# Optimization experiments

Hardware: AMD Instinct MI355X
Metric: run time of the kernel (lower is better)

## Reference

```python
import jax, jax.numpy as jnp
import numpy as np

EMBED_DIM = 1024
NUM_HEADS = 16
HEAD_DIM = EMBED_DIM // NUM_HEADS
B, S = 4, 2048


def setup_inputs() -> dict:
    key = jax.random.key(0)
    ks = jax.random.split(key, 12)
    s = 1.0 / np.sqrt(EMBED_DIM)
    inp = {
        'q': jax.random.normal(ks[0], (B, S, EMBED_DIM), jnp.float32),
        'k': jax.random.normal(ks[1], (B, S, EMBED_DIM), jnp.float32),
        'v': jax.random.normal(ks[2], (B, S, EMBED_DIM), jnp.float32),
        'mask': jnp.tril(jnp.ones((S, S), jnp.int32))[None, None],  # [1,1,S,S] causal
        'Wq': jax.random.normal(ks[3], (EMBED_DIM, EMBED_DIM), jnp.float32) * s,
        'bq': jax.random.normal(ks[4], (EMBED_DIM,), jnp.float32) * s,
        'Wk': jax.random.normal(ks[5], (EMBED_DIM, EMBED_DIM), jnp.float32) * s,
        'bk': jax.random.normal(ks[6], (EMBED_DIM,), jnp.float32) * s,
        'Wv': jax.random.normal(ks[7], (EMBED_DIM, EMBED_DIM), jnp.float32) * s,
        'bv': jax.random.normal(ks[8], (EMBED_DIM,), jnp.float32) * s,
        'Wo': jax.random.normal(ks[9], (EMBED_DIM, EMBED_DIM), jnp.float32) * s,
        'bo': jax.random.normal(ks[10], (EMBED_DIM,), jnp.float32) * s,
    }
    return inp


def _split(x):
    b, s, _ = x.shape
    return x.reshape(b, s, NUM_HEADS, HEAD_DIM).transpose(0, 2, 1, 3)  # [b,h,s,d]


def reference(q, k, v, mask, Wq, bq, Wk, bk, Wv, bv, Wo, bo):
    # torch Linear: x @ W.T + b
    Q = _split(q @ Wq.T + bq)
    K = _split(k @ Wk.T + bk)
    V = _split(v @ Wv.T + bv)
    scores = jnp.einsum('bhqd,bhkd->bhqk', Q, K) / np.sqrt(HEAD_DIM).astype(np.float32)
    scores = jnp.where(mask == 0, jnp.float32(-1e9), scores)
    attn = jax.nn.softmax(scores, axis=-1)  # dropout p=0.0 -> identity
    out = jnp.einsum('bhqk,bhkd->bhqd', attn, V)
    out = out.transpose(0, 2, 1, 3).reshape(q.shape[0], q.shape[1], EMBED_DIM)
    return out @ Wo.T + bo
```

## Files before the change

### kernel.cpp

```cpp
#include <hip/hip_runtime.h>

#define SEQ   2048
#define EMB   1024
#define NH    16
#define HD    64
#define BATCH 4

typedef __attribute__((ext_vector_type(8))) short short8;
typedef __attribute__((ext_vector_type(4))) float floatx4;

static __device__ __forceinline__ ushort f2bf_rne(float x) {
  unsigned u = __float_as_uint(x);
  unsigned r = u + 0x7FFFu + ((u >> 16) & 1u);
  return (ushort)(r >> 16);
}
static __device__ __forceinline__ float bf2f(ushort h) {
  return __uint_as_float(((unsigned)h) << 16);
}

static __device__ __forceinline__ void load16(const void* g, void* l) {
  __builtin_amdgcn_global_load_lds(
      (const __attribute__((address_space(1))) unsigned int*)g,
      (__attribute__((address_space(3))) unsigned int*)l, 16, 0, 0);
}

static __device__ __forceinline__ int swz_off(int row, int kg) {
  return (row >> 1) * 128 + (((row & 1) << 2) + (kg ^ ((row >> 1) & 3))) * 16;
}

static __device__ __forceinline__ void stage_tile(const ushort* __restrict__ g,
                                                  int row0, int k0,
                                                  ushort* lds, int t) {
#pragma unroll
  for (int i = 0; i < 2; ++i) {
    const int slot = t + i * 256;
    const int line = slot >> 3, s = slot & 7;
    const int row = line * 2 + (s >> 2);
    const int c = (s & 3) ^ (line & 3);
    load16(g + (size_t)(row0 + row) * EMB + k0 + c * 8, lds + slot * 8);
  }
}

__global__ __launch_bounds__(256) void wconv_kernel(const float* __restrict__ W,
                                                    ushort* __restrict__ Yh,
                                                    ushort* __restrict__ Yl) {
  const int i = (blockIdx.x * 256 + threadIdx.x) * 8;
  const float4 a = *(const float4*)(W + i);
  const float4 b = *(const float4*)(W + i + 4);
  const float xv[8] = {a.x, a.y, a.z, a.w, b.x, b.y, b.z, b.w};
  uint4 hp, lp;
  uint hw[8], lw[8];
#pragma unroll
  for (int j = 0; j < 8; ++j) {
    const ushort hh = f2bf_rne(xv[j]);
    hw[j] = hh;
    lw[j] = f2bf_rne(xv[j] - bf2f(hh));
  }
  hp.x = hw[0] | (hw[1] << 16); hp.y = hw[2] | (hw[3] << 16);
  hp.z = hw[4] | (hw[5] << 16); hp.w = hw[6] | (hw[7] << 16);
  lp.x = lw[0] | (lw[1] << 16); lp.y = lw[2] | (lw[3] << 16);
  lp.z = lw[4] | (lw[5] << 16); lp.w = lw[6] | (lw[7] << 16);
  *(uint4*)&Yh[i] = hp;
  *(uint4*)&Yl[i] = lp;
}

template <int MODE, bool PREA, bool PREB>
__global__ __launch_bounds__(256) void proj_mfma_kernel(
    const float* __restrict__ X, const ushort* __restrict__ Xh,
    const ushort* __restrict__ Xl, const float* __restrict__ W,
    const ushort* __restrict__ Wh, const ushort* __restrict__ Wl,
    const float* __restrict__ bias, float* __restrict__ Yf,
    ushort* __restrict__ Yh, ushort* __restrict__ Yl) {
  __shared__ ushort Ahi[PREA ? 128 * 32 : 128 * 40];
  __shared__ ushort Alo[PREA ? 128 * 32 : 128 * 40];
  __shared__ ushort Bhi[PREB ? 128 * 32 : 128 * 40];
  __shared__ ushort Blo[PREB ? 128 * 32 : 128 * 40];

  const int t = threadIdx.x;
  const int lane = t & 63, wave = t >> 6;
  const int m0 = blockIdx.y * 128, n0 = blockIdx.x * 128;
  const int wm = (wave >> 1) * 64, wn = (wave & 1) * 64;
  const int fr = lane & 15, kg = lane >> 4;

  floatx4 acc[4][4];
#pragma unroll
  for (int i = 0; i < 4; ++i)
#pragma unroll
    for (int j = 0; j < 4; ++j)
#pragma unroll
      for (int r = 0; r < 4; ++r) acc[i][j][r] = 0.f;

#pragma unroll 1
  for (int k0 = 0; k0 < EMB; k0 += 32) {
    __syncthreads();
    if constexpr (PREA) {
      stage_tile(Xh, m0, k0, Ahi, t);
      stage_tile(Xl, m0, k0, Alo, t);
    } else {
#pragma unroll
      for (int i = 0; i < 4; ++i) {
        const int f = t + 256 * i;
        const int row = f >> 3, kq = f & 7;
        const float4 a =
            *(const float4*)(X + (size_t)(m0 + row) * EMB + k0 + kq * 4);
        const ushort h0 = f2bf_rne(a.x), h1 = f2bf_rne(a.y);
        const ushort h2 = f2bf_rne(a.z), h3 = f2bf_rne(a.w);
        const ushort l0 = f2bf_rne(a.x - bf2f(h0)), l1 = f2bf_rne(a.y - bf2f(h1));
        const ushort l2 = f2bf_rne(a.z - bf2f(h2)), l3 = f2bf_rne(a.w - bf2f(h3));
        uint2 hp, lp;
        hp.x = (uint)h0 | ((uint)h1 << 16);
        hp.y = (uint)h2 | ((uint)h3 << 16);
        lp.x = (uint)l0 | ((uint)l1 << 16);
        lp.y = (uint)l2 | ((uint)l3 << 16);
        *(uint2*)&Ahi[row * 40 + kq * 4] = hp;
        *(uint2*)&Alo[row * 40 + kq * 4] = lp;
      }
    }
    if constexpr (PREB) {
      stage_tile(Wh, n0, k0, Bhi, t);
      stage_tile(Wl, n0, k0, Blo, t);
    } else {
#pragma unroll
      for (int i = 0; i < 4; ++i) {
        const int f = t + 256 * i;
        const int row = f >> 3, kq = f & 7;
        const float4 b =
            *(const float4*)(W + (size_t)(n0 + row) * EMB + k0 + kq * 4);
        const ushort h0 = f2bf_rne(b.x), h1 = f2bf_rne(b.y);
        const ushort h2 = f2bf_rne(b.z), h3 = f2bf_rne(b.w);
        const ushort l0 = f2bf_rne(b.x - bf2f(h0)), l1 = f2bf_rne(b.y - bf2f(h1));
        const ushort l2 = f2bf_rne(b.z - bf2f(h2)), l3 = f2bf_rne(b.w - bf2f(h3));
        uint2 hp, lp;
        hp.x = (uint)h0 | ((uint)h1 << 16);
        hp.y = (uint)h2 | ((uint)h3 << 16);
        lp.x = (uint)l0 | ((uint)l1 << 16);
        lp.y = (uint)l2 | ((uint)l3 << 16);
        *(uint2*)&Bhi[row * 40 + kq * 4] = hp;
        *(uint2*)&Blo[row * 40 + kq * 4] = lp;
      }
    }
    if constexpr (PREA || PREB) asm volatile("s_waitcnt vmcnt(0)");
    __syncthreads();

    short8 bhv[4], blv[4];
#pragma unroll
    for (int nf = 0; nf < 4; ++nf) {
      const int row = wn + nf * 16 + fr;
      if constexpr (PREB) {
        const int off = swz_off(row, kg);
        bhv[nf] = *(const short8*)((const char*)Bhi + off);
        blv[nf] = *(const short8*)((const char*)Blo + off);
      } else {
        bhv[nf] = *(const short8*)&Bhi[row * 40 + kg * 8];
        blv[nf] = *(const short8*)&Blo[row * 40 + kg * 8];
      }
    }
#pragma unroll
    for (int mf = 0; mf < 4; ++mf) {
      const int arow = wm + mf * 16 + fr;
      short8 ah, al;
      if constexpr (PREA) {
        const int off = swz_off(arow, kg);
        ah = *(const short8*)((const char*)Ahi + off);
        al = *(const short8*)((const char*)Alo + off);
      } else {
        ah = *(const short8*)&Ahi[arow * 40 + kg * 8];
        al = *(const short8*)&Alo[arow * 40 + kg * 8];
      }
#pragma unroll
      for (int nf = 0; nf < 4; ++nf) {
        acc[mf][nf] = __builtin_amdgcn_mfma_f32_16x16x32_bf16(ah, bhv[nf],
                                                              acc[mf][nf], 0, 0, 0);
        acc[mf][nf] = __builtin_amdgcn_mfma_f32_16x16x32_bf16(ah, blv[nf],
                                                              acc[mf][nf], 0, 0, 0);
        acc[mf][nf] = __builtin_amdgcn_mfma_f32_16x16x32_bf16(al, bhv[nf],
                                                              acc[mf][nf], 0, 0, 0);
      }
    }
  }

  const int rg = lane >> 4;
#pragma unroll
  for (int nf = 0; nf < 4; ++nf) {
    const int n = n0 + wn + nf * 16 + fr;
    const float bb = bias[n];
    if (MODE == 2) {
      const int hh = n >> 6, d = n & 63;
#pragma unroll
      for (int mf = 0; mf < 4; ++mf) {
        const int mb = m0 + wm + mf * 16 + rg * 4;
        const int b = mb >> 11, s = mb & (SEQ - 1);
        ushort4 hv, lv;
        {
          float v0 = acc[mf][nf][0] + bb, v1 = acc[mf][nf][1] + bb;
          float v2 = acc[mf][nf][2] + bb, v3 = acc[mf][nf][3] + bb;
          hv.x = f2bf_rne(v0); lv.x = f2bf_rne(v0 - bf2f(hv.x));
          hv.y = f2bf_rne(v1); lv.y = f2bf_rne(v1 - bf2f(hv.y));
          hv.z = f2bf_rne(v2); lv.z = f2bf_rne(v2 - bf2f(hv.z));
          hv.w = f2bf_rne(v3); lv.w = f2bf_rne(v3 - bf2f(hv.w));
        }
        const int idx = (b * NH + hh) * (HD * SEQ) + d * SEQ + s;
        *(ushort4*)&Yh[idx] = hv;
        *(ushort4*)&Yl[idx] = lv;
      }
    } else {
#pragma unroll
      for (int mf = 0; mf < 4; ++mf) {
#pragma unroll
        for (int r = 0; r < 4; ++r) {
          const int m = m0 + wm + mf * 16 + rg * 4 + r;
          float val = acc[mf][nf][r] + bb;
          if (MODE == 3) {
            Yf[(size_t)m * EMB + n] = val;
          } else {
            if (MODE == 0) val *= 0.125f;
            const int hh = n >> 6, d = n & 63;
            const int b = m >> 11, s = m & (SEQ - 1);
            const int idx = ((b * NH + hh) * SEQ + s) * HD + d;
            const ushort h = f2bf_rne(val);
            Yh[idx] = h;
            Yl[idx] = f2bf_rne(val - bf2f(h));
          }
        }
      }
    }
  }
}

template <bool SPLITOUT>
__global__ __launch_bounds__(256, 2) void attn_mfma_kernel(
    const ushort* __restrict__ Qh, const ushort* __restrict__ Ql,
    const ushort* __restrict__ Kh, const ushort* __restrict__ Kl,
    const ushort* __restrict__ Vth, const ushort* __restrict__ Vtl,
    float* __restrict__ O, ushort* __restrict__ Oh, ushort* __restrict__ Ol) {
  __shared__ __align__(16) ushort KHs[64 * 64], KLs[64 * 64];
  __shared__ __align__(16) ushort VHs[64 * 64], VLs[64 * 64];
  __shared__ __align__(16) ushort Phi[128 * 72], Plo[128 * 72];

  const int bh = blockIdx.x;
  const int qt = (gridDim.y - 1) - blockIdx.y;
  const int t = threadIdx.x;
  const int lane = t & 63, wave = t >> 6;
  const int fr = lane & 15, kg = lane >> 4;
  const int base = bh * (SEQ * HD);
  const int q0 = qt * 128 + wave * 32;

  short8 qh[2][2], ql[2][2];
#pragma unroll
  for (int mf = 0; mf < 2; ++mf)
#pragma unroll
    for (int ks = 0; ks < 2; ++ks) {
      const int idx = base + (q0 + mf * 16 + fr) * HD + ks * 32 + kg * 8;
      qh[mf][ks] = *(const short8*)&Qh[idx];
      ql[mf][ks] = *(const short8*)&Ql[idx];
    }

  floatx4 oacc[2][4];
  float m_run[2][4], l_run[2][4];
#pragma unroll
  for (int mf = 0; mf < 2; ++mf) {
#pragma unroll
    for (int nf = 0; nf < 4; ++nf)
#pragma unroll
      for (int r = 0; r < 4; ++r) oacc[mf][nf][r] = 0.f;
#pragma unroll
    for (int r = 0; r < 4; ++r) {
      m_run[mf][r] = -INFINITY;
      l_run[mf][r] = 0.f;
    }
  }

  const int nkt = 2 * qt + 2;
  const int r8 = lane >> 3, c8 = lane & 7;

#pragma unroll 1
  for (int kt = 0; kt < nkt; ++kt) {
    const int c0 = kt * 64;
    __syncthreads();

#pragma unroll
    for (int i = 0; i < 2; ++i) {
      const int row = wave * 16 + i * 8 + r8;
      const int sw = ((c8 ^ (row & 7)) << 3);
      const int gk = base + (c0 + row) * HD + sw;
      const int gv = base + row * SEQ + c0 + sw;
      ushort* lk = (ushort*)((char*)KHs + (wave * 16 + i * 8) * 128);
      ushort* lkl = (ushort*)((char*)KLs + (wave * 16 + i * 8) * 128);
      ushort* lv = (ushort*)((char*)VHs + (wave * 16 + i * 8) * 128);
      ushort* lvl = (ushort*)((char*)VLs + (wave * 16 + i * 8) * 128);
      load16(Kh + gk, lk);
      load16(Kl + gk, lkl);
      load16(Vth + gv, lv);
      load16(Vtl + gv, lvl);
    }
    asm volatile("s_waitcnt vmcnt(0)");
    __syncthreads();

    if (c0 > q0 + 31) continue;

    floatx4 s[2][4];
#pragma unroll
    for (int mf = 0; mf < 2; ++mf)
#pragma unroll
      for (int nf = 0; nf < 4; ++nf)
#pragma unroll
        for (int r = 0; r < 4; ++r) s[mf][nf][r] = 0.f;

#pragma unroll
    for (int ks = 0; ks < 2; ++ks)
#pragma unroll
      for (int nf = 0; nf < 4; ++nf) {
        const int row = nf * 16 + fr;
        const int byo = row * 128 + (((ks * 4 + kg) ^ (row & 7)) << 4);
        const short8 kh = *(const short8*)((const char*)KHs + byo);
        const short8 kl = *(const short8*)((const char*)KLs + byo);
#pragma unroll
        for (int mf = 0; mf < 2; ++mf) {
          s[mf][nf] = __builtin_amdgcn_mfma_f32_16x16x32_bf16(
              qh[mf][ks], kh, s[mf][nf], 0, 0, 0);
          s[mf][nf] = __builtin_amdgcn_mfma_f32_16x16x32_bf16(
              qh[mf][ks], kl, s[mf][nf], 0, 0, 0);
          s[mf][nf] = __builtin_amdgcn_mfma_f32_16x16x32_bf16(
              ql[mf][ks], kh, s[mf][nf], 0, 0, 0);
        }
      }

    if (c0 + 63 > q0) {
#pragma unroll
      for (int mf = 0; mf < 2; ++mf)
#pragma unroll
        for (int nf = 0; nf < 4; ++nf)
#pragma unroll
          for (int r = 0; r < 4; ++r) {
            const int row = q0 + mf * 16 + kg * 4 + r;
            const int col = c0 + nf * 16 + fr;
            if (col > row) s[mf][nf][r] = -1e9f;
          }
    }

#pragma unroll
    for (int mf = 0; mf < 2; ++mf)
#pragma unroll
      for (int r = 0; r < 4; ++r) {
        float v0 = s[mf][0][r], v1 = s[mf][1][r];
        float v2 = s[mf][2][r], v3 = s[mf][3][r];
        float tm = fmaxf(fmaxf(v0, v1), fmaxf(v2, v3));
        tm = fmaxf(tm, __shfl_xor(tm, 1));
        tm = fmaxf(tm, __shfl_xor(tm, 2));
        tm = fmaxf(tm, __shfl_xor(tm, 4));
        tm = fmaxf(tm, __shfl_xor(tm, 8));
        const float mnew = fmaxf(m_run[mf][r], tm);
        const float alpha = __expf(m_run[mf][r] - mnew);
        m_run[mf][r] = mnew;
        const float p0 = __expf(v0 - mnew), p1 = __expf(v1 - mnew);
        const float p2 = __expf(v2 - mnew), p3 = __expf(v3 - mnew);
        float rs = p0 + p1 + p2 + p3;
        rs += __shfl_xor(rs, 1);
        rs += __shfl_xor(rs, 2);
        rs += __shfl_xor(rs, 4);
        rs += __shfl_xor(rs, 8);
        l_run[mf][r] = l_run[mf][r] * alpha + rs;
        const int qrow = wave * 32 + mf * 16 + kg * 4 + r;
        const float pv[4] = {p0, p1, p2, p3};
#pragma unroll
        for (int nf = 0; nf < 4; ++nf) {
          const ushort h = f2bf_rne(pv[nf]);
          Phi[qrow * 72 + nf * 16 + fr] = h;
          Plo[qrow * 72 + nf * 16 + fr] = f2bf_rne(pv[nf] - bf2f(h));
        }
#pragma unroll
        for (int nf = 0; nf < 4; ++nf) oacc[mf][nf][r] *= alpha;
      }

#pragma unroll
    for (int ks = 0; ks < 2; ++ks) {
      short8 ph[2], pl[2];
#pragma unroll
      for (int mf = 0; mf < 2; ++mf) {
        const int qrow = wave * 32 + mf * 16 + fr;
        ph[mf] = *(const short8*)&Phi[qrow * 72 + ks * 32 + kg * 8];
        pl[mf] = *(const short8*)&Plo[qrow * 72 + ks * 32 + kg * 8];
      }
#pragma unroll
      for (int nf = 0; nf < 4; ++nf) {
        const int d = nf * 16 + fr;
        const int byo = d * 128 + (((ks * 4 + kg) ^ (d & 7)) << 4);
        const short8 vh = *(const short8*)((const char*)VHs + byo);
        const short8 vl = *(const short8*)((const char*)VLs + byo);
#pragma unroll
        for (int mf = 0; mf < 2; ++mf) {
          oacc[mf][nf] = __builtin_amdgcn_mfma_f32_16x16x32_bf16(
              ph[mf], vh, oacc[mf][nf], 0, 0, 0);
          oacc[mf][nf] = __builtin_amdgcn_mfma_f32_16x16x32_bf16(
              ph[mf], vl, oacc[mf][nf], 0, 0, 0);
          oacc[mf][nf] = __builtin_amdgcn_mfma_f32_16x16x32_bf16(
              pl[mf], vh, oacc[mf][nf], 0, 0, 0);
        }
      }
    }
  }

  const int b = bh >> 4, hsel = bh & 15;
#pragma unroll
  for (int mf = 0; mf < 2; ++mf)
#pragma unroll
    for (int r = 0; r < 4; ++r) {
      const int grow = q0 + mf * 16 + kg * 4 + r;
      const float inv = 1.f / l_run[mf][r];
      const int rowbase = (b * SEQ + grow) * EMB + hsel * HD;
#pragma unroll
      for (int nf = 0; nf < 4; ++nf) {
        const float val = oacc[mf][nf][r] * inv;
        const int idx = rowbase + nf * 16 + fr;
        if constexpr (SPLITOUT) {
          const ushort hh = f2bf_rne(val);
          Oh[idx] = hh;
          Ol[idx] = f2bf_rne(val - bf2f(hh));
        } else {
          O[idx] = val;
        }
      }
    }
}

extern "C" void kernel_launch(void* const* d_in, const int* in_sizes, int n_in,
                              void* d_out, int out_size, void* d_ws,
                              size_t ws_size, hipStream_t stream) {
  const float* q = (const float*)d_in[0];
  const float* k = (const float*)d_in[1];
  const float* v = (const float*)d_in[2];
  const float* Wq = (const float*)d_in[4];
  const float* bq = (const float*)d_in[5];
  const float* Wk = (const float*)d_in[6];
  const float* bk = (const float*)d_in[7];
  const float* Wv = (const float*)d_in[8];
  const float* bv = (const float*)d_in[9];
  const float* Wo = (const float*)d_in[10];
  const float* bo = (const float*)d_in[11];
  float* out = (float*)d_out;

  const size_t E = (size_t)BATCH * SEQ * EMB;
  const size_t WE = (size_t)EMB * EMB;
  ushort* us = (ushort*)d_ws;
  ushort* Qh = us;
  ushort* Ql = us + E;
  ushort* Kh = us + 2 * E;
  ushort* Kl = us + 3 * E;
  ushort* Vth = us + 4 * E;
  ushort* Vtl = us + 5 * E;

  const dim3 pgrid(EMB / 128, (BATCH * SEQ) / 128);
  const dim3 agrid(BATCH * NH, SEQ / 128);
  const dim3 blk(256);
  const int wgrid = (int)(WE / 8 / 256);

  if (ws_size >= 8 * E * sizeof(ushort)) {
    ushort* W3 = us + 6 * E;
    ushort* Wqh = W3, *Wql = W3 + WE;
    ushort* Wkh = W3 + 2 * WE, *Wkl = W3 + 3 * WE;
    ushort* Wvh = W3 + 4 * WE, *Wvl = W3 + 5 * WE;
    ushort* AOh = us + 6 * E, *AOl = us + 7 * E;
    ushort* Woh = us, *Wol = us + WE;

    wconv_kernel<<<wgrid, blk, 0, stream>>>(Wq, Wqh, Wql);
    wconv_kernel<<<wgrid, blk, 0, stream>>>(Wk, Wkh, Wkl);
    wconv_kernel<<<wgrid, blk, 0, stream>>>(Wv, Wvh, Wvl);
    proj_mfma_kernel<0, false, true><<<pgrid, blk, 0, stream>>>(
        q, nullptr, nullptr, nullptr, Wqh, Wql, bq, nullptr, Qh, Ql);
    proj_mfma_kernel<1, false, true><<<pgrid, blk, 0, stream>>>(
        k, nullptr, nullptr, nullptr, Wkh, Wkl, bk, nullptr, Kh, Kl);
    proj_mfma_kernel<2, false, true><<<pgrid, blk, 0, stream>>>(
        v, nullptr, nullptr, nullptr, Wvh, Wvl, bv, nullptr, Vth, Vtl);
    attn_mfma_kernel<true><<<agrid, blk, 0, stream>>>(Qh, Ql, Kh, Kl, Vth, Vtl,
                                                      nullptr, AOh, AOl);
    wconv_kernel<<<wgrid, blk, 0, stream>>>(Wo, Woh, Wol);
    proj_mfma_kernel<3, true, true><<<pgrid, blk, 0, stream>>>(
        nullptr, AOh, AOl, nullptr, Woh, Wol, bo, out, nullptr, nullptr);
  } else if (ws_size >= (6 * E + 6 * WE) * sizeof(ushort)) {
    ushort* W3 = us + 6 * E;
    ushort* Wqh = W3, *Wql = W3 + WE;
    ushort* Wkh = W3 + 2 * WE, *Wkl = W3 + 3 * WE;
    ushort* Wvh = W3 + 4 * WE, *Wvl = W3 + 5 * WE;
    ushort* AOh = (ushort*)d_out, *AOl = AOh + E;
    ushort* Woh = us, *Wol = us + WE;
    float* PO = (float*)(us + 2 * E);

    wconv_kernel<<<wgrid, blk, 0, stream>>>(Wq, Wqh, Wql);
    wconv_kernel<<<wgrid, blk, 0, stream>>>(Wk, Wkh, Wkl);
    wconv_kernel<<<wgrid, blk, 0, stream>>>(Wv, Wvh, Wvl);
    proj_mfma_kernel<0, false, true><<<pgrid, blk, 0, stream>>>(
        q, nullptr, nullptr, nullptr, Wqh, Wql, bq, nullptr, Qh, Ql);
    proj_mfma_kernel<1, false, true><<<pgrid, blk, 0, stream>>>(
        k, nullptr, nullptr, nullptr, Wkh, Wkl, bk, nullptr, Kh, Kl);
    proj_mfma_kernel<2, false, true><<<pgrid, blk, 0, stream>>>(
        v, nullptr, nullptr, nullptr, Wvh, Wvl, bv, nullptr, Vth, Vtl);
    attn_mfma_kernel<true><<<agrid, blk, 0, stream>>>(Qh, Ql, Kh, Kl, Vth, Vtl,
                                                      nullptr, AOh, AOl);
    wconv_kernel<<<wgrid, blk, 0, stream>>>(Wo, Woh, Wol);
    proj_mfma_kernel<3, true, true><<<pgrid, blk, 0, stream>>>(
        nullptr, AOh, AOl, nullptr, Woh, Wol, bo, PO, nullptr, nullptr);
    hipMemcpyAsync(out, PO, E * sizeof(float), hipMemcpyDeviceToDevice, stream);
  } else {
    float* AO = out;
    float* PO = (float*)d_ws;
    proj_mfma_kernel<0, false, false><<<pgrid, blk, 0, stream>>>(
        q, nullptr, nullptr, Wq, nullptr, nullptr, bq, nullptr, Qh, Ql);
    proj_mfma_kernel<1, false, false><<<pgrid, blk, 0, stream>>>(
        k, nullptr, nullptr, Wk, nullptr, nullptr, bk, nullptr, Kh, Kl);
    proj_mfma_kernel<2, false, false><<<pgrid, blk, 0, stream>>>(
        v, nullptr, nullptr, Wv, nullptr, nullptr, bv, nullptr, Vth, Vtl);
    attn_mfma_kernel<false><<<agrid, blk, 0, stream>>>(
        Qh, Ql, Kh, Kl, Vth, Vtl, AO, nullptr, nullptr);
    proj_mfma_kernel<3, false, false><<<pgrid, blk, 0, stream>>>(
        AO, nullptr, nullptr, Wo, nullptr, nullptr, bo, PO, nullptr, nullptr);
    hipMemcpyAsync(out, PO, E * sizeof(float), hipMemcpyDeviceToDevice, stream);
  }
}
```

Before: 438.4 us.

## Compute transposed S tile so P stays in registers, drop LDS P staging

```diff
diff --git a/kernel.cpp b/kernel.cpp
--- a/kernel.cpp
+++ b/kernel.cpp
@@ -228,14 +228,13 @@
 }
 
 template <bool SPLITOUT>
-__global__ __launch_bounds__(256, 2) void attn_mfma_kernel(
+__global__ __launch_bounds__(256, 4) void attn_mfma_kernel(
     const ushort* __restrict__ Qh, const ushort* __restrict__ Ql,
     const ushort* __restrict__ Kh, const ushort* __restrict__ Kl,
     const ushort* __restrict__ Vth, const ushort* __restrict__ Vtl,
     float* __restrict__ O, ushort* __restrict__ Oh, ushort* __restrict__ Ol) {
   __shared__ __align__(16) ushort KHs[64 * 64], KLs[64 * 64];
   __shared__ __align__(16) ushort VHs[64 * 64], VLs[64 * 64];
-  __shared__ __align__(16) ushort Phi[128 * 72], Plo[128 * 72];
 
   const int bh = blockIdx.x;
   const int qt = (gridDim.y - 1) - blockIdx.y;
@@ -256,18 +255,15 @@
     }
 
   floatx4 oacc[2][4];
-  float m_run[2][4], l_run[2][4];
+  float m_run[2], l_run[2];
 #pragma unroll
   for (int mf = 0; mf < 2; ++mf) {
 #pragma unroll
     for (int nf = 0; nf < 4; ++nf)
 #pragma unroll
       for (int r = 0; r < 4; ++r) oacc[mf][nf][r] = 0.f;
-#pragma unroll
-    for (int r = 0; r < 4; ++r) {
-      m_run[mf][r] = -INFINITY;
-      l_run[mf][r] = 0.f;
-    }
+    m_run[mf] = -INFINITY;
+    l_run[mf] = 0.f;
   }
 
   const int nkt = 2 * qt + 2;
@@ -298,30 +294,30 @@
 
     if (c0 > q0 + 31) continue;
 
-    floatx4 s[2][4];
+    floatx4 s2[2][4];
 #pragma unroll
     for (int mf = 0; mf < 2; ++mf)
 #pragma unroll
       for (int nf = 0; nf < 4; ++nf)
 #pragma unroll
-        for (int r = 0; r < 4; ++r) s[mf][nf][r] = 0.f;
-
-#pragma unroll
-    for (int ks = 0; ks < 2; ++ks)
+        for (int r = 0; r < 4; ++r) s2[mf][nf][r] = 0.f;
+
+#pragma unroll
+    for (int ksd = 0; ksd < 2; ++ksd)
 #pragma unroll
       for (int nf = 0; nf < 4; ++nf) {
-        const int row = nf * 16 + fr;
-        const int byo = row * 128 + (((ks * 4 + kg) ^ (row & 7)) << 4);
+        const int kr = 32 * (nf >> 1) + 8 * (fr >> 2) + 4 * (nf & 1) + (fr & 3);
+        const int byo = kr * 128 + (((ksd * 4 + kg) ^ (kr & 7)) << 4);
         const short8 kh = *(const short8*)((const char*)KHs + byo);
         const short8 kl = *(const short8*)((const char*)KLs + byo);
 #pragma unroll
         for (int mf = 0; mf < 2; ++mf) {
-          s[mf][nf] = __builtin_amdgcn_mfma_f32_16x16x32_bf16(
-              qh[mf][ks], kh, s[mf][nf], 0, 0, 0);
-          s[mf][nf] = __builtin_amdgcn_mfma_f32_16x16x32_bf16(
-              qh[mf][ks], kl, s[mf][nf], 0, 0, 0);
-          s[mf][nf] = __builtin_amdgcn_mfma_f32_16x16x32_bf16(
-              ql[mf][ks], kh, s[mf][nf], 0, 0, 0);
+          s2[mf][nf] = __builtin_amdgcn_mfma_f32_16x16x32_bf16(
+              kh, qh[mf][ksd], s2[mf][nf], 0, 0, 0);
+          s2[mf][nf] = __builtin_amdgcn_mfma_f32_16x16x32_bf16(
+              kh, ql[mf][ksd], s2[mf][nf], 0, 0, 0);
+          s2[mf][nf] = __builtin_amdgcn_mfma_f32_16x16x32_bf16(
+              kl, qh[mf][ksd], s2[mf][nf], 0, 0, 0);
         }
       }
 
@@ -332,55 +328,68 @@
         for (int nf = 0; nf < 4; ++nf)
 #pragma unroll
           for (int r = 0; r < 4; ++r) {
-            const int row = q0 + mf * 16 + kg * 4 + r;
-            const int col = c0 + nf * 16 + fr;
-            if (col > row) s[mf][nf][r] = -1e9f;
+            const int col = c0 + 32 * (nf >> 1) + 8 * kg + 4 * (nf & 1) + r;
+            const int row = q0 + mf * 16 + fr;
+            if (col > row) s2[mf][nf][r] = -1e9f;
           }
     }
 
+    float alpha2[2];
+#pragma unroll
+    for (int mf = 0; mf < 2; ++mf) {
+      float pm = s2[mf][0][0];
+#pragma unroll
+      for (int nf = 0; nf < 4; ++nf)
+#pragma unroll
+        for (int r = 0; r < 4; ++r) pm = fmaxf(pm, s2[mf][nf][r]);
+      pm = fmaxf(pm, __shfl_xor(pm, 16));
+      pm = fmaxf(pm, __shfl_xor(pm, 32));
+      const float mnew = fmaxf(m_run[mf], pm);
+      const float al = __expf(m_run[mf] - mnew);
+      m_run[mf] = mnew;
+      float sum = 0.f;
+#pragma unroll
+      for (int nf = 0; nf < 4; ++nf)
+#pragma unroll
+        for (int r = 0; r < 4; ++r) {
+          const float p = __expf(s2[mf][nf][r] - mnew);
+          s2[mf][nf][r] = p;
+          sum += p;
+        }
+      sum += __shfl_xor(sum, 16);
+      sum += __shfl_xor(sum, 32);
+      l_run[mf] = l_run[mf] * al + sum;
+      alpha2[mf] = al;
+    }
+
 #pragma unroll
     for (int mf = 0; mf < 2; ++mf)
 #pragma unroll
       for (int r = 0; r < 4; ++r) {
-        float v0 = s[mf][0][r], v1 = s[mf][1][r];
-        float v2 = s[mf][2][r], v3 = s[mf][3][r];
-        float tm = fmaxf(fmaxf(v0, v1), fmaxf(v2, v3));
-        tm = fmaxf(tm, __shfl_xor(tm, 1));
-        tm = fmaxf(tm, __shfl_xor(tm, 2));
-        tm = fmaxf(tm, __shfl_xor(tm, 4));
-        tm = fmaxf(tm, __shfl_xor(tm, 8));
-        const float mnew = fmaxf(m_run[mf][r], tm);
-        const float alpha = __expf(m_run[mf][r] - mnew);
-        m_run[mf][r] = mnew;
-        const float p0 = __expf(v0 - mnew), p1 = __expf(v1 - mnew);
-        const float p2 = __expf(v2 - mnew), p3 = __expf(v3 - mnew);
-        float rs = p0 + p1 + p2 + p3;
-        rs += __shfl_xor(rs, 1);
-        rs += __shfl_xor(rs, 2);
-        rs += __shfl_xor(rs, 4);
-        rs += __shfl_xor(rs, 8);
-        l_run[mf][r] = l_run[mf][r] * alpha + rs;
-        const int qrow = wave * 32 + mf * 16 + kg * 4 + r;
-        const float pv[4] = {p0, p1, p2, p3};
-#pragma unroll
-        for (int nf = 0; nf < 4; ++nf) {
-          const ushort h = f2bf_rne(pv[nf]);
-          Phi[qrow * 72 + nf * 16 + fr] = h;
-          Plo[qrow * 72 + nf * 16 + fr] = f2bf_rne(pv[nf] - bf2f(h));
-        }
-#pragma unroll
-        for (int nf = 0; nf < 4; ++nf) oacc[mf][nf][r] *= alpha;
-      }
-
-#pragma unroll
-    for (int ks = 0; ks < 2; ++ks) {
-      short8 ph[2], pl[2];
-#pragma unroll
-      for (int mf = 0; mf < 2; ++mf) {
-        const int qrow = wave * 32 + mf * 16 + fr;
-        ph[mf] = *(const short8*)&Phi[qrow * 72 + ks * 32 + kg * 8];
-        pl[mf] = *(const short8*)&Plo[qrow * 72 + ks * 32 + kg * 8];
-      }
+        const float a = __shfl(alpha2[mf], (kg * 4 + r) | (lane & 48));
+#pragma unroll
+        for (int nf = 0; nf < 4; ++nf) oacc[mf][nf][r] *= a;
+      }
+
+    short8 pah[2][2], pal[2][2];
+#pragma unroll
+    for (int mf = 0; mf < 2; ++mf)
+#pragma unroll
+      for (int ks = 0; ks < 2; ++ks) {
+        short8 h, l;
+#pragma unroll
+        for (int j = 0; j < 8; ++j) {
+          const float v = s2[mf][2 * ks + (j >> 2)][j & 3];
+          const ushort hh = f2bf_rne(v);
+          h[j] = (short)hh;
+          l[j] = (short)f2bf_rne(v - bf2f(hh));
+        }
+        pah[mf][ks] = h;
+        pal[mf][ks] = l;
+      }
+
+#pragma unroll
+    for (int ks = 0; ks < 2; ++ks)
 #pragma unroll
       for (int nf = 0; nf < 4; ++nf) {
         const int d = nf * 16 + fr;
@@ -390,14 +399,13 @@
 #pragma unroll
         for (int mf = 0; mf < 2; ++mf) {
           oacc[mf][nf] = __builtin_amdgcn_mfma_f32_16x16x32_bf16(
-              ph[mf], vh, oacc[mf][nf], 0, 0, 0);
+              pah[mf][ks], vh, oacc[mf][nf], 0, 0, 0);
           oacc[mf][nf] = __builtin_amdgcn_mfma_f32_16x16x32_bf16(
-              ph[mf], vl, oacc[mf][nf], 0, 0, 0);
+              pah[mf][ks], vl, oacc[mf][nf], 0, 0, 0);
           oacc[mf][nf] = __builtin_amdgcn_mfma_f32_16x16x32_bf16(
-              pl[mf], vh, oacc[mf][nf], 0, 0, 0);
-        }
-      }
-    }
+              pal[mf][ks], vh, oacc[mf][nf], 0, 0, 0);
+        }
+      }
   }
 
   const int b = bh >> 4, hsel = bh & 15;
@@ -405,8 +413,9 @@
   for (int mf = 0; mf < 2; ++mf)
 #pragma unroll
     for (int r = 0; r < 4; ++r) {
+      const float lv = __shfl(l_run[mf], (kg * 4 + r) | (lane & 48));
+      const float inv = 1.f / lv;
       const int grow = q0 + mf * 16 + kg * 4 + r;
-      const float inv = 1.f / l_run[mf][r];
       const int rowbase = (b * SEQ + grow) * EMB + hsel * HD;
 #pragma unroll
       for (int nf = 0; nf < 4; ++nf) {
```

Measured after the change: 457.6 us. 4.4% more time.
